# Optimization experiments

Hardware: AMD Instinct MI355X
Metric: run time of the kernel (lower is better)

## Reference

```python
import jax, jax.numpy as jnp
import numpy as np

N_NODES = 10000
N_EDGES = 160000
C = 16        # num_feature_channels
C2 = 8        # output channels per irrep per head (C/2)
HID = 64      # radial_network_hidden_units
NH = 2        # num_attention_heads
NG = 16       # graphs in batch
F_IN = 64     # num_features
F_OUT = 32    # number_of_output_features
HEAD_TYPES = ("normal", "inverse")  # invariant_dictionary
IRREP_SLICES = ((0, 1), (1, 4), (4, 9))  # l=0,1,2 blocks of the SH dim


def _sph_harm(r):
    """Component-normalized real spherical harmonics l=0..2 for unit vectors r [E,3] -> [E,9]."""
    x, y, z = r[:, 0], r[:, 1], r[:, 2]
    c3 = 1.7320508   # sqrt(3)
    c15 = 3.8729833  # sqrt(15)
    l0 = jnp.ones_like(x)[:, None]
    l1 = c3 * r
    l2 = jnp.stack([
        c15 * x * y,
        c15 * y * z,
        1.1180340 * (2.0 * z * z - x * x - y * y),  # sqrt(5)/2
        c15 * x * z,
        1.9364917 * (x * x - y * y),                 # sqrt(15)/2
    ], axis=-1)
    return jnp.concatenate([l0, l1, l2], axis=-1)


def setup_inputs() -> dict:
    key = jax.random.key(0)
    ks = jax.random.split(key, 16)
    node_features = jax.random.normal(ks[0], (N_NODES, F_IN), jnp.float32)
    pos = jax.random.normal(ks[1], (N_NODES, 3), jnp.float32)
    src = jax.random.randint(ks[2], (N_EDGES,), 0, N_NODES)
    off = jax.random.randint(ks[3], (N_EDGES,), 1, N_NODES)  # avoid self-loops (d=0)
    tgt = (src + off) % N_NODES
    edge_index = jnp.stack([src, tgt], axis=0)
    batch = jnp.sort(jax.random.randint(ks[4], (N_NODES,), 0, NG))
    s = lambda k, shape, fan: (jax.random.normal(k, shape, jnp.float32) / np.sqrt(fan)).astype(jnp.float32)
    return dict(
        node_features=node_features, pos=pos,
        W_embed=s(ks[5], (F_IN, C), F_IN), b_embed=jnp.zeros((C,), jnp.float32),
        Wq=s(ks[6], (NH, C, C), C), Wk=s(ks[7], (NH, C, C), C),
        W1=s(ks[8], (NH, 1, HID), 1), b1=jnp.zeros((NH, HID), jnp.float32),
        Wa=s(ks[9], (NH, HID), HID), Wv=s(ks[10], (NH, HID, C * 3), HID),
        Wo=s(ks[11], (NH, 3, C, C2), C),
        Wproj=s(ks[12], (NH * C2, F_OUT), NH * C2), bproj=jnp.zeros((F_OUT,), jnp.float32),
        edge_index=edge_index, batch=batch,
    )


def _forward(node_features, pos, W_embed, b_embed, Wq, Wk, W1, b1, Wa, Wv, Wo,
             Wproj, bproj, edge_index, batch):
    src, tgt = edge_index[0], edge_index[1]
    rel = pos[tgt] - pos[src]                       # [E,3]
    dist = jnp.linalg.norm(rel, axis=-1, keepdims=True)  # [E,1]
    rhat = rel / dist
    Y = _sph_harm(rhat)                             # [E,9]
    x = node_features @ W_embed + b_embed          # [N,C] scalar (0e) features
    xs = x[src]                                     # [E,C]
    inv_sqrt_c = 1.0 / np.sqrt(C)
    head_outs = []
    for h in range(NH):
        d_feat = dist if HEAD_TYPES[h] == "normal" else dist ** -2  # [E,1]
        hid = jax.nn.relu(d_feat @ W1[h] + b1[h])   # [E,HID] radial network
        att_bias = hid @ Wa[h]                      # [E]
        wv = (hid @ Wv[h]).reshape(-1, C, 3)        # [E,C,3] per-(channel,l) radial weights
        q = x @ Wq[h]
        k = x @ Wk[h]
        logit = jnp.sum(q[tgt] * k[src], axis=-1) * inv_sqrt_c + att_bias  # [E]
        # segment softmax over incoming edges of each target node
        m = jax.ops.segment_max(logit, tgt, num_segments=N_NODES)
        e = jnp.exp(logit - m[tgt])
        z = jax.ops.segment_sum(e, tgt, num_segments=N_NODES)
        alpha = e / z[tgt]                          # [E]
        # expand per-l weights to per-m: dims (1,3,5)
        wv_m = jnp.repeat(wv, np.array([1, 3, 5]), axis=2, total_repeat_length=9)  # [E,C,9]
        msg = (alpha[:, None, None] * wv_m) * xs[:, :, None] * Y[:, None, :]       # [E,C,9]
        node_out = jax.ops.segment_sum(msg, tgt, num_segments=N_NODES)             # [N,C,9]
        parts = [jnp.einsum('ncm,co->nom', node_out[:, :, s0:s1], Wo[h, li]).reshape(N_NODES, -1)
                 for li, (s0, s1) in enumerate(IRREP_SLICES)]
        head_outs.append(jnp.concatenate(parts, axis=-1))  # [N, C2*9]
    feat = jnp.concatenate(head_outs, axis=-1)              # [N, NH*C2*9]
    pooled = jax.ops.segment_sum(feat, batch, num_segments=NG)  # [NG, NH*C2*9]
    # equivariant Linear -> F_OUT x 0e: only scalar (l=0) components map to scalars
    blk = C2 * 9
    scal = jnp.concatenate([pooled[:, h * blk: h * blk + C2] for h in range(NH)], axis=-1)  # [NG, NH*C2]
    return scal @ Wproj + bproj                             # [NG, F_OUT]


def reference(node_features, pos, W_embed, b_embed, Wq, Wk, W1, b1, Wa, Wv, Wo,
              Wproj, bproj, edge_index, batch):
    return _forward(node_features, pos, W_embed, b_embed, Wq, Wk, W1, b1, Wa, Wv,
                    Wo, Wproj, bproj, edge_index, batch)
```

## Files before the change

### kernel.cpp

```cpp
#include <hip/hip_runtime.h>
#include <math.h>

#define NN 10000
#define NE 160000
#define CAP 96

__device__ __forceinline__ unsigned bf16pack2(float a, float b) {
    unsigned ua = __float_as_uint(a);
    unsigned ub = __float_as_uint(b);
    ua = ua + 0x7fffu + ((ua >> 16) & 1u);
    ub = ub + 0x7fffu + ((ub >> 16) & 1u);
    return (ua >> 16) | (ub & 0xffff0000u);
}

__global__ __launch_bounds__(256) void k_xqk(const float* __restrict__ nf,
        const float* __restrict__ We, const float* __restrict__ be,
        const float* __restrict__ Wq, const float* __restrict__ Wk,
        const float* __restrict__ Wv,
        float* __restrict__ x, float* __restrict__ q, float* __restrict__ k,
        int* __restrict__ zeroReg, float* __restrict__ vC) {
    int t = threadIdx.x;
    int gid = blockIdx.x * 256 + t;
    if (gid < 10272) zeroReg[gid] = 0;
    if (blockIdx.x == 0) {
        for (int i = t; i < 2048; i += 256) {
            int h = i >> 10, j = (i >> 4) & 63, c = i & 15;
            vC[i] = Wv[(h * 64 + j) * 48 + 3 * c];
        }
    }
    __shared__ float sWe[64 * 16];
    __shared__ float sWq[2 * 16 * 16];
    __shared__ float sWk[2 * 16 * 16];
    __shared__ float sNF[16 * 64];
    __shared__ float sX[16 * 16];
    for (int i = t; i < 1024; i += 256) sWe[i] = We[i];
    for (int i = t; i < 512; i += 256) { sWq[i] = Wq[i]; sWk[i] = Wk[i]; }
    int nodeBase = blockIdx.x * 16;
    for (int i = t; i < 1024; i += 256) {
        int n = nodeBase + (i >> 6);
        sNF[i] = (n < NN) ? nf[n * 64 + (i & 63)] : 0.0f;
    }
    __syncthreads();
    int ln = t >> 4, c = t & 15;
    int n = nodeBase + ln;
    float acc = be[c];
    #pragma unroll 16
    for (int j = 0; j < 64; ++j) acc = fmaf(sNF[ln * 64 + j], sWe[j * 16 + c], acc);
    sX[ln * 16 + c] = acc;
    __syncthreads();
    if (n < NN) {
        x[n * 16 + c] = acc;
        #pragma unroll
        for (int h = 0; h < 2; ++h) {
            float aq = 0.0f, ak = 0.0f;
            #pragma unroll
            for (int j = 0; j < 16; ++j) {
                float xv = sX[ln * 16 + j];
                aq = fmaf(xv, sWq[(h * 16 + j) * 16 + c], aq);
                ak = fmaf(xv, sWk[(h * 16 + j) * 16 + c], ak);
            }
            q[(n * 2 + h) * 16 + c] = aq;
            k[(n * 2 + h) * 16 + c] = ak;
        }
    }
}

__global__ __launch_bounds__(256) void k_edge(const float* __restrict__ pos,
        const int* __restrict__ ei,
        const float* __restrict__ q, const float* __restrict__ k,
        const float* __restrict__ W1, const float* __restrict__ b1,
        const float* __restrict__ Wa, const float* __restrict__ vC,
        const float* __restrict__ Wo,
        const float* __restrict__ x, int* __restrict__ deg,
        float* __restrict__ lgp, uint4* __restrict__ gb) {
    int e = blockIdx.x * 256 + threadIdx.x;
    if (e >= NE) return;
    int s = ei[e], t = ei[NE + e];
    int p = atomicAdd(&deg[t], 1);
    bool ok = (p < CAP);
    size_t slot = (size_t)t * CAP + p;
    float dx = pos[t * 3 + 0] - pos[s * 3 + 0];
    float dy = pos[t * 3 + 1] - pos[s * 3 + 1];
    float dz = pos[t * 3 + 2] - pos[s * 3 + 2];
    float d = sqrtf(dx * dx + dy * dy + dz * dz);
    float fh[2] = { d, 1.0f / (d * d) };
    const float4* xp = (const float4*)(x + (size_t)s * 16);
    float4 xs0 = xp[0], xs1 = xp[1], xs2 = xp[2], xs3 = xp[3];
    float xf[16] = { xs0.x, xs0.y, xs0.z, xs0.w, xs1.x, xs1.y, xs1.z, xs1.w,
                     xs2.x, xs2.y, xs2.z, xs2.w, xs3.x, xs3.y, xs3.z, xs3.w };
    float L2v[2];
    #pragma unroll
    for (int h = 0; h < 2; ++h) {
        const float4* qt = (const float4*)(q + (size_t)t * 32 + h * 16);
        const float4* ks = (const float4*)(k + (size_t)s * 32 + h * 16);
        float4 a0 = qt[0], a1 = qt[1], a2 = qt[2], a3 = qt[3];
        float4 b0 = ks[0], c1 = ks[1], c2 = ks[2], c3 = ks[3];
        float dot = a0.x * b0.x + a0.y * b0.y + a0.z * b0.z + a0.w * b0.w
                  + a1.x * c1.x + a1.y * c1.y + a1.z * c1.z + a1.w * c1.w
                  + a2.x * c2.x + a2.y * c2.y + a2.z * c2.z + a2.w * c2.w
                  + a3.x * c3.x + a3.y * c3.y + a3.z * c3.z + a3.w * c3.w;
        float f = fh[h];
        float att = 0.0f;
        float acc[16];
        #pragma unroll
        for (int c = 0; c < 16; ++c) acc[c] = 0.0f;
        const float* w1b = W1 + h * 64;
        const float* b1b = b1 + h * 64;
        const float* wab = Wa + h * 64;
        const float* vcb = vC + h * 1024;
        #pragma unroll 8
        for (int j = 0; j < 64; ++j) {
            float hid = fmaxf(fmaf(f, w1b[j], b1b[j]), 0.0f);
            att = fmaf(hid, wab[j], att);
            #pragma unroll
            for (int c = 0; c < 16; ++c)
                acc[c] = fmaf(hid, vcb[j * 16 + c], acc[c]);
        }
        L2v[h] = fmaf(dot, 0.25f, att);
        float g[8];
        #pragma unroll
        for (int o = 0; o < 8; ++o) g[o] = 0.0f;
        const float* wob = Wo + h * 384;
        #pragma unroll
        for (int c = 0; c < 16; ++c) {
            float axc = acc[c] * xf[c];
            #pragma unroll
            for (int o = 0; o < 8; ++o) g[o] = fmaf(axc, wob[c * 8 + o], g[o]);
        }
        if (ok) {
            gb[slot * 2 + h] = make_uint4(bf16pack2(g[0], g[1]), bf16pack2(g[2], g[3]),
                                          bf16pack2(g[4], g[5]), bf16pack2(g[6], g[7]));
        }
    }
    if (ok) *(float2*)(lgp + slot * 2) = make_float2(L2v[0], L2v[1]);
}

__global__ __launch_bounds__(256) void k_gather(const int* __restrict__ deg,
        const float* __restrict__ lgp, const unsigned* __restrict__ gb,
        float* __restrict__ feat) {
    int t0 = threadIdx.x;
    int wv = t0 >> 6;
    int lane = t0 & 63;
    int pid = blockIdx.x * 4 + wv;
    int n = pid >> 1, h = pid & 1;
    int dg = min(deg[n], CAP);
    int g = lane >> 2, p = lane & 3;
    float m = -INFINITY, z = 0.0f, u0 = 0.0f, u1 = 0.0f;
    const float* lgb = lgp + (size_t)n * (CAP * 2) + h;
    const unsigned* gbb = gb + (size_t)n * (CAP * 8) + h * 4 + p;
    for (int i = g; i < dg; i += 16) {
        float L = lgb[i * 2];
        unsigned wbits = gbb[(size_t)i * 8];
        float ga = __uint_as_float(wbits << 16);
        float gbv = __uint_as_float(wbits & 0xffff0000u);
        float nm = fmaxf(m, L);
        float sc = (m > -INFINITY) ? __expf(m - nm) : 0.0f;
        float w  = __expf(L - nm);
        u0 = fmaf(u0, sc, w * ga);
        u1 = fmaf(u1, sc, w * gbv);
        z  = fmaf(z, sc, w);
        m = nm;
    }
    #pragma unroll
    for (int off = 4; off <= 32; off <<= 1) {
        float mo = __shfl_xor(m, off, 64);
        float zo = __shfl_xor(z, off, 64);
        float a0o = __shfl_xor(u0, off, 64);
        float a1o = __shfl_xor(u1, off, 64);
        float nm = fmaxf(m, mo);
        float a = (m  > -INFINITY) ? __expf(m  - nm) : 0.0f;
        float b = (mo > -INFINITY) ? __expf(mo - nm) : 0.0f;
        u0 = u0 * a + a0o * b;
        u1 = u1 * a + a1o * b;
        z  = z * a + zo * b;
        m = nm;
    }
    if (lane < 4) {
        float inv = (z > 0.0f) ? 1.0f / z : 0.0f;
        *(float2*)(feat + n * 16 + h * 8 + p * 2) = make_float2(u0 * inv, u1 * inv);
    }
}

__global__ __launch_bounds__(256) void k_poolfinal(const float* __restrict__ feat,
        const int* __restrict__ batch, float* __restrict__ pooled,
        int* __restrict__ done, const float* __restrict__ Wproj,
        const float* __restrict__ bproj, float* __restrict__ out) {
    __shared__ float sP[256];
    int t = threadIdx.x;
    sP[t] = 0.0f;
    __syncthreads();
    int tid = blockIdx.x * 256 + t;
    int c = tid & 15, seg = tid >> 4;
    int n0 = seg * 16, n1 = min(n0 + 16, NN);
    float run = 0.0f;
    int curg = -1;
    for (int n = n0; n < n1; ++n) {
        int gg = batch[n];
        if (gg != curg) {
            if (curg >= 0) atomicAdd(&sP[curg * 16 + c], run);
            run = 0.0f; curg = gg;
        }
        run += feat[n * 16 + c];
    }
    if (curg >= 0) atomicAdd(&sP[curg * 16 + c], run);
    __syncthreads();
    atomicAdd(&pooled[t], sP[t]);
    __threadfence();
    __shared__ int lastBlk;
    if (t == 0) lastBlk = (atomicAdd(done, 1) == 39) ? 1 : 0;
    __syncthreads();
    if (!lastBlk) return;
    __shared__ float sPool[256];
    sPool[t] = atomicAdd(&pooled[t], 0.0f);
    __syncthreads();
    for (int i = t; i < 512; i += 256) {
        int g = i >> 5, fo = i & 31;
        float acc = bproj[fo];
        #pragma unroll
        for (int j = 0; j < 16; ++j) acc = fmaf(sPool[g * 16 + j], Wproj[j * 32 + fo], acc);
        out[g * 32 + fo] = acc;
    }
}

extern "C" void kernel_launch(void* const* d_in, const int* in_sizes, int n_in,
                              void* d_out, int out_size, void* d_ws, size_t ws_size,
                              hipStream_t stream) {
    const float* nf    = (const float*)d_in[0];
    const float* pos   = (const float*)d_in[1];
    const float* We    = (const float*)d_in[2];
    const float* be    = (const float*)d_in[3];
    const float* Wq    = (const float*)d_in[4];
    const float* Wk    = (const float*)d_in[5];
    const float* W1    = (const float*)d_in[6];
    const float* b1    = (const float*)d_in[7];
    const float* Wa    = (const float*)d_in[8];
    const float* Wv    = (const float*)d_in[9];
    const float* Wo    = (const float*)d_in[10];
    const float* Wproj = (const float*)d_in[11];
    const float* bproj = (const float*)d_in[12];
    const int*   ei    = (const int*)d_in[13];
    const int*   batch = (const int*)d_in[14];
    float* out = (float*)d_out;
    (void)in_sizes; (void)n_in; (void)out_size; (void)ws_size;

    float* ws     = (float*)d_ws;
    float* x      = ws;
    float* q      = x + 160000;
    float* k      = q + 320000;
    float* feat   = k + 320000;
    float* pooled = feat + 160000;
    int*   deg    = (int*)(pooled + 256);
    int*   done   = deg + 10000;
    float* vC     = (float*)(done + 16);
    float* lgp    = vC + 2048;
    unsigned* gbu = (unsigned*)(lgp + (size_t)NN * CAP * 2);

    hipLaunchKernelGGL(k_xqk,      dim3(625),  dim3(256), 0, stream,
                       nf, We, be, Wq, Wk, Wv, x, q, k, (int*)pooled, vC);
    hipLaunchKernelGGL(k_edge,     dim3(625),  dim3(256), 0, stream,
                       pos, ei, q, k, W1, b1, Wa, vC, Wo, x, deg, lgp, (uint4*)gbu);
    hipLaunchKernelGGL(k_gather,   dim3(5000), dim3(256), 0, stream,
                       deg, lgp, gbu, feat);
    hipLaunchKernelGGL(k_poolfinal, dim3(40),  dim3(256), 0, stream,
                       feat, batch, pooled, done, Wproj, bproj, out);
}
```

Baseline: 131.8 us.

## Fuse graph pooling and final projection into the gather kernel

The separate pooling kernel is removed. Each gather wavefront now atomically adds its normalized per-node head output straight into the per-graph pooled buffer, indexed by the node's batch id. The last of the 5000 blocks, found with a done counter, runs the final projection. This drops one kernel launch and the write and read of the feat array. In exchange it adds many global float atomics on only 256 addresses, which may contend, and makes the floating-point summation order nondeterministic.

Result: slower. 446.7 us (+239.0%).

```diff
diff --git a/kernel.cpp b/kernel.cpp
--- a/kernel.cpp
+++ b/kernel.cpp
@@ -135,9 +135,11 @@
     if (ok) *(float2*)(lgp + slot * 2) = make_float2(L2v[0], L2v[1]);
 }
 
-__global__ __launch_bounds__(256) void k_gather(const int* __restrict__ deg,
+__global__ __launch_bounds__(256) void k_gatherpool(const int* __restrict__ deg,
         const float* __restrict__ lgp, const unsigned* __restrict__ gb,
-        float* __restrict__ feat) {
+        const int* __restrict__ batch, float* __restrict__ pooled,
+        int* __restrict__ done, const float* __restrict__ Wproj,
+        const float* __restrict__ bproj, float* __restrict__ out) {
     int t0 = threadIdx.x;
     int wv = t0 >> 6;
     int lane = t0 & 63;
@@ -177,48 +179,26 @@
     }
     if (lane < 4) {
         float inv = (z > 0.0f) ? 1.0f / z : 0.0f;
-        *(float2*)(feat + n * 16 + h * 8 + p * 2) = make_float2(u0 * inv, u1 * inv);
-    }
-}
-
-__global__ __launch_bounds__(256) void k_poolfinal(const float* __restrict__ feat,
-        const int* __restrict__ batch, float* __restrict__ pooled,
-        int* __restrict__ done, const float* __restrict__ Wproj,
-        const float* __restrict__ bproj, float* __restrict__ out) {
-    __shared__ float sP[256];
-    int t = threadIdx.x;
-    sP[t] = 0.0f;
-    __syncthreads();
-    int tid = blockIdx.x * 256 + t;
-    int c = tid & 15, seg = tid >> 4;
-    int n0 = seg * 16, n1 = min(n0 + 16, NN);
-    float run = 0.0f;
-    int curg = -1;
-    for (int n = n0; n < n1; ++n) {
-        int gg = batch[n];
-        if (gg != curg) {
-            if (curg >= 0) atomicAdd(&sP[curg * 16 + c], run);
-            run = 0.0f; curg = gg;
-        }
-        run += feat[n * 16 + c];
-    }
-    if (curg >= 0) atomicAdd(&sP[curg * 16 + c], run);
-    __syncthreads();
-    atomicAdd(&pooled[t], sP[t]);
+        int grp = batch[n];
+        float* dst = pooled + grp * 16 + h * 8 + p * 2;
+        atomicAdd(dst + 0, u0 * inv);
+        atomicAdd(dst + 1, u1 * inv);
+    }
     __threadfence();
+    __syncthreads();
     __shared__ int lastBlk;
-    if (t == 0) lastBlk = (atomicAdd(done, 1) == 39) ? 1 : 0;
+    if (t0 == 0) lastBlk = (atomicAdd(done, 1) == 4999) ? 1 : 0;
     __syncthreads();
     if (!lastBlk) return;
     __shared__ float sPool[256];
-    sPool[t] = atomicAdd(&pooled[t], 0.0f);
-    __syncthreads();
-    for (int i = t; i < 512; i += 256) {
-        int g = i >> 5, fo = i & 31;
+    sPool[t0] = atomicAdd(&pooled[t0], 0.0f);
+    __syncthreads();
+    for (int i = t0; i < 512; i += 256) {
+        int gq = i >> 5, fo = i & 31;
         float acc = bproj[fo];
         #pragma unroll
-        for (int j = 0; j < 16; ++j) acc = fmaf(sPool[g * 16 + j], Wproj[j * 32 + fo], acc);
-        out[g * 32 + fo] = acc;
+        for (int j = 0; j < 16; ++j) acc = fmaf(sPool[gq * 16 + j], Wproj[j * 32 + fo], acc);
+        out[gq * 32 + fo] = acc;
     }
 }
 
@@ -247,20 +227,17 @@
     float* x      = ws;
     float* q      = x + 160000;
     float* k      = q + 320000;
-    float* feat   = k + 320000;
-    float* pooled = feat + 160000;
+    float* pooled = k + 320000;
     int*   deg    = (int*)(pooled + 256);
     int*   done   = deg + 10000;
     float* vC     = (float*)(done + 16);
     float* lgp    = vC + 2048;
     unsigned* gbu = (unsigned*)(lgp + (size_t)NN * CAP * 2);
 
-    hipLaunchKernelGGL(k_xqk,      dim3(625),  dim3(256), 0, stream,
+    hipLaunchKernelGGL(k_xqk,       dim3(625),  dim3(256), 0, stream,
                        nf, We, be, Wq, Wk, Wv, x, q, k, (int*)pooled, vC);
-    hipLaunchKernelGGL(k_edge,     dim3(625),  dim3(256), 0, stream,
+    hipLaunchKernelGGL(k_edge,      dim3(625),  dim3(256), 0, stream,
                        pos, ei, q, k, W1, b1, Wa, vC, Wo, x, deg, lgp, (uint4*)gbu);
-    hipLaunchKernelGGL(k_gather,   dim3(5000), dim3(256), 0, stream,
-                       deg, lgp, gbu, feat);
-    hipLaunchKernelGGL(k_poolfinal, dim3(40),  dim3(256), 0, stream,
-                       feat, batch, pooled, done, Wproj, bproj, out);
-}
+    hipLaunchKernelGGL(k_gatherpool, dim3(5000), dim3(256), 0, stream,
+                       deg, lgp, gbu, batch, pooled, done, Wproj, bproj, out);
+}
```
